# Kernel tuning notes

Hardware: AMD Instinct MI355X
Metric: run time of the kernel (lower is better)

Reference implementation:

```python
import jax, jax.numpy as jnp
import numpy as np

N, FIN, C1, C2 = 4096, 6, 1000, 1000
K1, K2, KR = 3, 6, 3
NR, S, NCLS = 20, 205, 40


def pairwise_adj(x):
    # exp(-squared_euclidean_distance), RGCNN pairwise_distance
    inner = -2.0 * jnp.einsum('bnf,bmf->bnm', x, x)
    sq = jnp.sum(x * x, axis=-1, keepdims=True)
    return jnp.exp(-(sq + inner + jnp.swapaxes(sq, 1, 2)))


def knn_sparsify(adj, k):
    # keep top-k similarities per row, zero the rest (get_one_matrix_knn)
    vals, idx = jax.lax.top_k(adj, k)
    B, n, _ = adj.shape
    b = jnp.arange(B)[:, None, None]
    r = jnp.arange(n)[None, :, None]
    return jnp.zeros_like(adj).at[b, r, idx].set(vals)


def get_laplacian(W):
    # normalized Laplacian L = I - D^-1/2 W D^-1/2
    dinv = 1.0 / jnp.sqrt(jnp.sum(W, axis=-1))
    Lnorm = W * dinv[:, :, None] * dinv[:, None, :]
    return jnp.eye(W.shape[-1], dtype=W.dtype)[None] - Lnorm


def cheb_conv(x, L, W, b, K):
    # Chebyshev recursion: Tx0=x, Tx1=Lx, Txk=2L Tx_{k-1} - Tx_{k-2}
    Tx = [x]
    if K > 1:
        Tx.append(jnp.einsum('bnm,bmf->bnf', L, x))
    for _ in range(2, K):
        Tx.append(2.0 * jnp.einsum('bnm,bmf->bnf', L, Tx[-1]) - Tx[-2])
    xhat = jnp.concatenate(Tx, axis=-1)  # [B, N, K*Fin]
    return jnp.einsum('bnf,fo->bno', xhat, W) + b


def setup_inputs() -> dict:
    key = jax.random.key(0)
    ks = jax.random.split(key, 16)
    sc = 0.02
    return {
        'x': jax.random.normal(ks[0], (1, N, FIN), jnp.float32),
        'k': 40,
        'batch_size': 1,
        'num_points': N,
        'vertices_Reeb': jax.random.normal(ks[1], (NR, 3), jnp.float32),
        'laplacian_Reeb': jax.random.normal(ks[2], (NR, NR), jnp.float32),
        'sccs': jax.random.randint(ks[3], (NR, S), 0, N),
        'W1': jax.random.normal(ks[4], (K1 * FIN, C1), jnp.float32) * sc,
        'b1': jnp.zeros((C1,), jnp.float32),
        'W2': jax.random.normal(ks[5], (K2 * C1, C2), jnp.float32) * sc,
        'b2': jnp.zeros((C2,), jnp.float32),
        'Wr': jax.random.normal(ks[6], (KR * C1, C2), jnp.float32) * sc,
        'br': jnp.zeros((C2,), jnp.float32),
        'fc1_w': jax.random.normal(ks[7], (2 * C2, 512), jnp.float32) * sc,
        'fc1_b': jnp.zeros((512,), jnp.float32),
        'fc2_w': jax.random.normal(ks[8], (512, 128), jnp.float32) * sc,
        'fc2_b': jnp.zeros((128,), jnp.float32),
        'fc3_w': jax.random.normal(ks[9], (128, NCLS), jnp.float32) * sc,
        'fc3_b': jnp.zeros((NCLS,), jnp.float32),
    }


def reference(x, k, batch_size, num_points, vertices_Reeb, laplacian_Reeb, sccs,
              W1, b1, W2, b2, Wr, br, fc1_w, fc1_b, fc2_w, fc2_b, fc3_w, fc3_b):
    fro = lambda a: jnp.linalg.norm(a.reshape(-1))
    regs = []
    # dynamic KNN graph + Laplacian (no_grad in original -> stop_gradient)
    L = jax.lax.stop_gradient(get_laplacian(knn_sparsify(pairwise_adj(x), k)))
    out = jax.nn.relu(cheb_conv(x, L, W1, b1, K1))  # [1, N, 1000]
    regs.append(fro(jnp.einsum('bnc,bnm,bmf->bcf', out, L, x)))
    # Reeb pooling: max over each scc's node features (sample 0)
    vfr = jnp.max(out[0][sccs], axis=1)[None]  # [1, 20, 1000]
    L_reeb = laplacian_Reeb[None]
    # second dynamic graph on features
    L2 = jax.lax.stop_gradient(get_laplacian(knn_sparsify(pairwise_adj(out), k)))
    out2 = jax.nn.relu(cheb_conv(out, L2, W2, b2, K2))
    regs.append(fro(jnp.einsum('bnc,bnm,bmf->bcf', out2, L2, x)))
    out_reeb = jax.nn.relu(cheb_conv(vfr, L_reeb, Wr, br, KR))
    out_m = jnp.max(out2, axis=1)       # [1, 1000]
    reeb_m = jnp.max(out_reeb, axis=1)  # [1, 1000]
    of = jnp.concatenate([reeb_m, out_m], axis=1)  # [1, 2000]
    of = jax.nn.relu(of @ fc1_w + fc1_b)
    regs += [jnp.linalg.norm(fc1_w.T[0]) ** 2, fc1_b[0] ** 2]
    of = jax.nn.relu(of @ fc2_w + fc2_b)
    regs += [jnp.linalg.norm(fc2_w.T[0]) ** 2, fc2_b[0] ** 2]
    of = of @ fc3_w + fc3_b  # [1, 40]
    regs += [jnp.linalg.norm(fc3_w.T[0]) ** 2, fc3_b[0] ** 2]
    return of, jnp.stack(regs)
```

## Files before the change

kernel.cpp:

```cpp
#include <hip/hip_runtime.h>
#include <math.h>

#define N4    4096
#define FDIM  6
#define CC    1000
#define KP    1024
#define KP6   (6 * KP)
#define KNN   40
#define NRB   20
#define SSC   205

typedef __attribute__((ext_vector_type(8))) short bf16x8;
typedef __attribute__((ext_vector_type(4))) float f32x4;

__device__ __forceinline__ unsigned short f2bf(float f) {
    unsigned u = __float_as_uint(f);
    u = (u + 0x7fffu + ((u >> 16) & 1u)) >> 16;
    return (unsigned short)u;
}
__device__ __forceinline__ float bf2f(short s) {
    return __uint_as_float(((unsigned)(unsigned short)s) << 16);
}

__device__ __forceinline__ unsigned d2key(float d) {
    unsigned u = __float_as_uint(d);
    return ((int)u < 0) ? u : (~u) ^ 0x80000000u;
}
__device__ __forceinline__ float key2d(unsigned k) {
    unsigned u = (k >> 31) ? k : (~k) ^ 0x80000000u;
    return __uint_as_float(u);
}

__device__ __forceinline__ void gload16(const unsigned short* g, short* l) {
    __builtin_amdgcn_global_load_lds(
        (const __attribute__((address_space(1))) unsigned int*)g,
        (__attribute__((address_space(3))) unsigned int*)l, 16, 0, 0);
}


__global__ __launch_bounds__(256) void sqx_kernel(const float* __restrict__ x,
                                                  float* __restrict__ sq1,
                                                  float* __restrict__ xhat) {
    int n = blockIdx.x * blockDim.x + threadIdx.x;
    if (n >= N4) return;
    float s = 0.f;
#pragma unroll
    for (int f = 0; f < FDIM; ++f) {
        float v = x[n * FDIM + f];
        s += v * v;
        xhat[n * 18 + f] = v;
    }
    sq1[n] = s;
}


#define NHC 8
#define HSTRIDE 257

struct TopkSh {
    unsigned sv[N4];
    int hist[NHC * HSTRIDE];
    int sc[256];
    float red[8];
    unsigned short cidx[N4];
    unsigned s_pfx;
    int s_need, s_cnt, s_m;
};

__device__ __forceinline__ void hist_pick(TopkSh& sh, int level, int t, int lane, int w, int nc) {
    if (t < 256) {
        int cnt = 0;
        for (int c = 0; c < nc; ++c) cnt += sh.hist[c * HSTRIDE + t];
        sh.sc[t] = cnt;
    }
    __syncthreads();
    if (w == 0) {
        int need = sh.s_need;
        unsigned pfx = sh.s_pfx;
        int c0 = sh.sc[4 * lane + 0], c1 = sh.sc[4 * lane + 1];
        int c2 = sh.sc[4 * lane + 2], c3 = sh.sc[4 * lane + 3];
        int s = c0 + c1 + c2 + c3;
        int suf = s;
#pragma unroll
        for (int off = 1; off < 64; off <<= 1) {
            int ov = __shfl_down(suf, off, 64);
            if (lane + off < 64) suf += ov;
        }
        int above = suf - s;
        int i3 = above + c3, i2 = i3 + c2, i1 = i2 + c1, i0 = i1 + c0;
        if (i3 >= need && i3 - c3 < need) { sh.s_need = need - (i3 - c3); sh.s_pfx = pfx | ((unsigned)(4 * lane + 3) << level); }
        if (i2 >= need && i2 - c2 < need) { sh.s_need = need - (i2 - c2); sh.s_pfx = pfx | ((unsigned)(4 * lane + 2) << level); }
        if (i1 >= need && i1 - c1 < need) { sh.s_need = need - (i1 - c1); sh.s_pfx = pfx | ((unsigned)(4 * lane + 1) << level); }
        if (i0 >= need && i0 - c0 < need) { sh.s_need = need - (i0 - c0); sh.s_pfx = pfx | ((unsigned)(4 * lane + 0) << level); }
    }
    __syncthreads();
}

__device__ void topk_select(TopkSh& sh, int n, int* __restrict__ idx,
                            float* __restrict__ val, float* __restrict__ rowsum) {
    int t = threadIdx.x, lane = t & 63, w = t >> 6;
    if (t == 0) { sh.s_pfx = 0u; sh.s_need = KNN; sh.s_cnt = 0; sh.s_m = 0; }
    for (int q = t; q < NHC * HSTRIDE; q += 512) sh.hist[q] = 0;
    __syncthreads();
    int* hw = &sh.hist[(t & 7) * HSTRIDE];

    {
        unsigned prevb = 0xFFFFFFFFu; int rl = 0;
        for (int i = t; i < N4; i += 512) {
            unsigned b = sh.sv[i] >> 24;
            if (b == prevb) ++rl;
            else { if (rl) atomicAdd(&hw[prevb], rl); prevb = b; rl = 1; }
        }
        if (rl) atomicAdd(&hw[prevb], rl);
    }
    __syncthreads();
    hist_pick(sh, 24, t, lane, w, NHC);
    unsigned b1 = sh.s_pfx >> 24;

    for (int i = t; i < N4; i += 512) {
        unsigned u = sh.sv[i];
        bool isc = ((u >> 24) >= b1);
        unsigned long long mm = __ballot(isc);
        int cw = __popcll(mm);
        int base = 0;
        if (lane == 0 && cw) base = atomicAdd(&sh.s_m, cw);
        base = __shfl(base, 0);
        if (isc) sh.cidx[base + __popcll(mm & ((1ull << lane) - 1ull))] = (unsigned short)i;
    }
    __syncthreads();
    int mcnt = sh.s_m;

    for (int level = 16; level >= 0; level -= 8) {
        for (int q = t; q < HSTRIDE; q += 512) sh.hist[q] = 0;
        __syncthreads();
        unsigned pfx = sh.s_pfx;
        for (int j = t; j < mcnt; j += 512) {
            unsigned u = sh.sv[sh.cidx[j]];
            if ((u >> (level + 8)) == (pfx >> (level + 8)))
                atomicAdd(&sh.hist[(u >> level) & 255], 1);
        }
        __syncthreads();
        hist_pick(sh, level, t, lane, w, 1);
    }
    unsigned Tbits = sh.s_pfx;
    float Tf = __expf(-key2d(Tbits));
    int needEq = sh.s_need;

    float psum = 0.f;
    for (int j = t; j < mcnt; j += 512) {
        unsigned u = sh.sv[sh.cidx[j]];
        if (u > Tbits) {
            int p = atomicAdd(&sh.s_cnt, 1);
            float v = __expf(-key2d(u));
            idx[(size_t)n * KNN + p] = (int)sh.cidx[j];
            val[(size_t)n * KNN + p] = v;
            psum += v;
        }
    }
#pragma unroll
    for (int o = 32; o; o >>= 1) psum += __shfl_down(psum, o);
    if (lane == 0) sh.red[w] = psum;
    __syncthreads();
    if (t == 0) {
        float s = 0.f;
#pragma unroll
        for (int q = 0; q < 8; ++q) s += sh.red[q];
        rowsum[n] = s + (float)needEq * Tf;
    }

    if (t < 64) {
        int filled = KNN - needEq;
        for (int ib = 0; ib < N4 && filled < KNN; ib += 64) {
            bool eq = (sh.sv[ib + t] == Tbits);
            unsigned long long m = __ballot(eq);
            int pre = __popcll(m & ((1ull << t) - 1ull));
            if (eq && (filled + pre) < KNN) {
                idx[(size_t)n * KNN + filled + pre] = ib + t;
                val[(size_t)n * KNN + filled + pre] = Tf;
            }
            filled += __popcll(m);
        }
    }
}

__global__ __launch_bounds__(512) void topk_fused1(const float* __restrict__ x,
                                                   const float* __restrict__ sq1,
                                                   int* __restrict__ idx, float* __restrict__ val,
                                                   float* __restrict__ rowsum) {
    __shared__ TopkSh sh;
    __shared__ float xn[FDIM];
    __shared__ float sns;
    int n = blockIdx.x;
    int t = threadIdx.x;
    if (t < FDIM) xn[t] = x[n * FDIM + t];
    if (t == FDIM) sns = sq1[n];
    __syncthreads();
    float x0 = xn[0], x1 = xn[1], x2 = xn[2], x3 = xn[3], x4 = xn[4], x5 = xn[5];
    float sn = sns;
    for (int i = t; i < N4; i += 512) {
        const float2* xi = (const float2*)(x + i * FDIM);
        float2 p0 = xi[0], p1 = xi[1], p2 = xi[2];
        float d = x0 * p0.x + x1 * p0.y + x2 * p1.x + x3 * p1.y + x4 * p2.x + x5 * p2.y;
        float e = sn + sq1[i] - 2.f * d;
        sh.sv[i] = d2key(e);
    }
    topk_select(sh, n, idx, val, rowsum);
}

__global__ __launch_bounds__(512) void topk_radix(const unsigned short* __restrict__ S,
                                                  int* __restrict__ idx, float* __restrict__ val,
                                                  float* __restrict__ rowsum) {
    __shared__ TopkSh sh;
    int n = blockIdx.x;
    int t = threadIdx.x;
    const unsigned short* row = S + (size_t)n * N4;
    bf16x8 a = *(const bf16x8*)(row + 8 * t);
#pragma unroll
    for (int q = 0; q < 8; ++q) sh.sv[8 * t + q] = d2key(bf2f(a[q]));
    topk_select(sh, n, idx, val, rowsum);
}

__global__ __launch_bounds__(256) void wnorm_kernel(float* __restrict__ wv,
                                                    const int* __restrict__ idx,
                                                    const float* __restrict__ rs) {
    int i = blockIdx.x * 256 + threadIdx.x;
    if (i >= N4 * KNN) return;
    int n = i / KNN;
    wv[i] = wv[i] * rsqrtf(rs[n]) * rsqrtf(rs[idx[i]]);
}

__global__ __launch_bounds__(64) void spmv_cheb(const float* __restrict__ Tc,
                                                const float* __restrict__ Tp,
                                                float* __restrict__ Tn,
                                                const int* __restrict__ idx,
                                                const float* __restrict__ wv,
                                                int F, int sC, int sP, int sN,
                                                float a, float b) {
    __shared__ int   si[KNN];
    __shared__ float sw[KNN];
    int n = blockIdx.x;
    if (threadIdx.x < KNN) {
        si[threadIdx.x] = idx[(size_t)n * KNN + threadIdx.x];
        sw[threadIdx.x] = wv[(size_t)n * KNN + threadIdx.x];
    }
    __syncthreads();
    for (int c = threadIdx.x; c < F; c += blockDim.x) {
        float s = 0.f;
#pragma unroll 8
        for (int j = 0; j < KNN; ++j) s += sw[j] * Tc[(size_t)si[j] * sC + c];
        float v = a * (Tc[(size_t)n * sC + c] - s);
        if (b != 0.f) v -= b * Tp[(size_t)n * sP + c];
        Tn[(size_t)n * sN + c] = v;
    }
}

__global__ __launch_bounds__(256) void spmv_cheb_bf(const unsigned short* __restrict__ Tcbf,
                                                    const unsigned short* __restrict__ Tpbf,
                                                    unsigned short* __restrict__ Tnbf,
                                                    const int* __restrict__ idx,
                                                    const float* __restrict__ wv,
                                                    float a, float b) {
    __shared__ int   si[KNN];
    __shared__ float sw[KNN];
    __shared__ float part[128][8];
    int n = blockIdx.x;
    int t = threadIdx.x;
    int tt = t & 127, h = t >> 7;
    if (t < KNN) {
        si[t] = idx[(size_t)n * KNN + t];
        sw[t] = wv[(size_t)n * KNN + t];
    }
    __syncthreads();
    int c = tt * 8;
    float acc0 = 0, acc1 = 0, acc2 = 0, acc3 = 0, acc4 = 0, acc5 = 0, acc6 = 0, acc7 = 0;
    int j0 = h * 20;
#pragma unroll 4
    for (int j = j0; j < j0 + 20; ++j) {
        bf16x8 v = *(const bf16x8*)(Tcbf + (size_t)si[j] * KP6 + c);
        float wj = sw[j];
        acc0 += wj * bf2f(v[0]); acc1 += wj * bf2f(v[1]);
        acc2 += wj * bf2f(v[2]); acc3 += wj * bf2f(v[3]);
        acc4 += wj * bf2f(v[4]); acc5 += wj * bf2f(v[5]);
        acc6 += wj * bf2f(v[6]); acc7 += wj * bf2f(v[7]);
    }
    if (h == 1) {
        part[tt][0] = acc0; part[tt][1] = acc1; part[tt][2] = acc2; part[tt][3] = acc3;
        part[tt][4] = acc4; part[tt][5] = acc5; part[tt][6] = acc6; part[tt][7] = acc7;
    }
    __syncthreads();
    if (h == 0) {
        acc0 += part[tt][0]; acc1 += part[tt][1]; acc2 += part[tt][2]; acc3 += part[tt][3];
        acc4 += part[tt][4]; acc5 += part[tt][5]; acc6 += part[tt][6]; acc7 += part[tt][7];
        bf16x8 tc = *(const bf16x8*)(Tcbf + (size_t)n * KP6 + c);
        float o0 = a * (bf2f(tc[0]) - acc0), o1 = a * (bf2f(tc[1]) - acc1);
        float o2 = a * (bf2f(tc[2]) - acc2), o3 = a * (bf2f(tc[3]) - acc3);
        float o4 = a * (bf2f(tc[4]) - acc4), o5 = a * (bf2f(tc[5]) - acc5);
        float o6 = a * (bf2f(tc[6]) - acc6), o7 = a * (bf2f(tc[7]) - acc7);
        if (b != 0.f) {
            bf16x8 tp = *(const bf16x8*)(Tpbf + (size_t)n * KP6 + c);
            o0 -= b * bf2f(tp[0]); o1 -= b * bf2f(tp[1]);
            o2 -= b * bf2f(tp[2]); o3 -= b * bf2f(tp[3]);
            o4 -= b * bf2f(tp[4]); o5 -= b * bf2f(tp[5]);
            o6 -= b * bf2f(tp[6]); o7 -= b * bf2f(tp[7]);
        }
        bf16x8 ob;
        ob[0] = (short)f2bf(o0); ob[1] = (short)f2bf(o1);
        ob[2] = (short)f2bf(o2); ob[3] = (short)f2bf(o3);
        ob[4] = (short)f2bf(o4); ob[5] = (short)f2bf(o5);
        ob[6] = (short)f2bf(o6); ob[7] = (short)f2bf(o7);
        *(bf16x8*)(Tnbf + (size_t)n * KP6 + c) = ob;
    }
}


__global__ __launch_bounds__(256) void cvt_bf16_kernel(const float* __restrict__ in,
                                                       unsigned short* __restrict__ out) {
    int i = blockIdx.x * 256 + threadIdx.x;
    int r = i >> 7, g = i & 127;
    bf16x8 v;
    if (g < 125) {
        float4 a = *(const float4*)(in + (size_t)r * CC + g * 8);
        float4 b = *(const float4*)(in + (size_t)r * CC + g * 8 + 4);
        v[0] = (short)f2bf(a.x); v[1] = (short)f2bf(a.y);
        v[2] = (short)f2bf(a.z); v[3] = (short)f2bf(a.w);
        v[4] = (short)f2bf(b.x); v[5] = (short)f2bf(b.y);
        v[6] = (short)f2bf(b.z); v[7] = (short)f2bf(b.w);
    } else {
#pragma unroll
        for (int q = 0; q < 8; ++q) v[q] = 0;
    }
    *(bf16x8*)(out + (size_t)r * KP6 + g * 8) = v;
}

__global__ __launch_bounds__(256) void w2t_kernel(const float* __restrict__ W2,
                                                  unsigned short* __restrict__ out) {
    __shared__ unsigned short tile[64][65];
    int t = threadIdx.x;
    int k0 = blockIdx.x * 64, n0 = blockIdx.y * 64, s = blockIdx.z;
#pragma unroll
    for (int p = 0; p < 16; ++p) {
        int i = p * 256 + t;
        int kk = i >> 6, nn = i & 63;
        int k = k0 + kk, n = n0 + nn;
        float v = (k < CC && n < CC) ? W2[((size_t)s * CC + k) * CC + n] : 0.f;
        tile[kk][nn] = f2bf(v);
    }
    __syncthreads();
#pragma unroll
    for (int p = 0; p < 16; ++p) {
        int i = p * 256 + t;
        int nn = i >> 6, kk = i & 63;
        out[(size_t)(n0 + nn) * KP6 + (size_t)s * KP + k0 + kk] = tile[kk][nn];
    }
}


#define LDT 32
#define SP2 136
#define SP 264
#define ABUF (128 * LDT)
#define BBUF (256 * LDT)

template<int STR>
__device__ __forceinline__ void gemm_core128(const unsigned short* __restrict__ Ag,
                                             const unsigned short* __restrict__ Bg,
                                             short* As, short* Bs, int t,
                                             int kbeg, int kend,
                                             f32x4 (&acc)[4][4]) {
    int l = t & 63, w = t >> 6;
    int wm = (w >> 1) * 64, wn = (w & 1) * 64;
    int lr = l & 15, lq8 = (l >> 4) * 8;
    size_t soff = (size_t)(16 * w + (l >> 2)) * STR + (l & 3) * 8;
    const unsigned short* gA = Ag + soff;
    const unsigned short* gB = Bg + soff;
    int wb = w * 512;
    gload16(gA + kbeg, As + wb);
    gload16(gA + kbeg + (size_t)64 * STR, As + wb + 64 * LDT);
    gload16(gB + kbeg, Bs + wb);
    gload16(gB + kbeg + (size_t)64 * STR, Bs + wb + 64 * LDT);
    __syncthreads();
    int cur = 0;
    for (int k0 = kbeg; k0 < kend; k0 += 32) {
        int nxt = cur ^ 1;
        if (k0 + 32 < kend) {
            short* nA = As + nxt * ABUF + wb;
            short* nB = Bs + nxt * ABUF + wb;
            gload16(gA + k0 + 32, nA);
            gload16(gA + k0 + 32 + (size_t)64 * STR, nA + 64 * LDT);
            gload16(gB + k0 + 32, nB);
            gload16(gB + k0 + 32 + (size_t)64 * STR, nB + 64 * LDT);
        }
        const short* cA = As + cur * ABUF;
        const short* cB = Bs + cur * ABUF;
        bf16x8 af[4], bfr[4];
#pragma unroll
        for (int mi = 0; mi < 4; ++mi)
            af[mi] = *(const bf16x8*)&cA[(wm + mi * 16 + lr) * LDT + lq8];
#pragma unroll
        for (int ni = 0; ni < 4; ++ni)
            bfr[ni] = *(const bf16x8*)&cB[(wn + ni * 16 + lr) * LDT + lq8];
#pragma unroll
        for (int mi = 0; mi < 4; ++mi)
#pragma unroll
            for (int ni = 0; ni < 4; ++ni)
                acc[mi][ni] = __builtin_amdgcn_mfma_f32_16x16x32_bf16(af[mi], bfr[ni], acc[mi][ni], 0, 0, 0);
        __syncthreads();
        cur = nxt;
    }
}

template<int STR>
__device__ __forceinline__ void gemm_core256(const unsigned short* __restrict__ Ag,
                                             const unsigned short* __restrict__ Bg,
                                             short* As, short* Bs, int t,
                                             int kbeg, int kend,
                                             f32x4 (&acc)[4][8]) {
    int l = t & 63, w = t >> 6;
    int wm = (w >> 1) * 64, wn = (w & 1) * 128;
    int lr = l & 15, lq8 = (l >> 4) * 8;
    size_t soff = (size_t)(16 * w + (l >> 2)) * STR + (l & 3) * 8;
    const unsigned short* gA = Ag + soff;
    const unsigned short* gB = Bg + soff;
    int wb = w * 512;
    gload16(gA + kbeg, As + wb);
    gload16(gA + kbeg + (size_t)64 * STR, As + wb + 64 * LDT);
    gload16(gB + kbeg, Bs + wb);
    gload16(gB + kbeg + (size_t)64 * STR, Bs + wb + 64 * LDT);
    gload16(gB + kbeg + (size_t)128 * STR, Bs + wb + 128 * LDT);
    gload16(gB + kbeg + (size_t)192 * STR, Bs + wb + 192 * LDT);
    __syncthreads();
    int cur = 0;
    for (int k0 = kbeg; k0 < kend; k0 += 32) {
        int nxt = cur ^ 1;
        if (k0 + 32 < kend) {
            short* nA = As + nxt * ABUF + wb;
            short* nB = Bs + nxt * BBUF + wb;
            gload16(gA + k0 + 32, nA);
            gload16(gA + k0 + 32 + (size_t)64 * STR, nA + 64 * LDT);
            gload16(gB + k0 + 32, nB);
            gload16(gB + k0 + 32 + (size_t)64 * STR, nB + 64 * LDT);
            gload16(gB + k0 + 32 + (size_t)128 * STR, nB + 128 * LDT);
            gload16(gB + k0 + 32 + (size_t)192 * STR, nB + 192 * LDT);
        }
        const short* cA = As + cur * ABUF;
        const short* cB = Bs + cur * BBUF;
        bf16x8 af[4], bfr[8];
#pragma unroll
        for (int mi = 0; mi < 4; ++mi)
            af[mi] = *(const bf16x8*)&cA[(wm + mi * 16 + lr) * LDT + lq8];
#pragma unroll
        for (int ni = 0; ni < 8; ++ni)
            bfr[ni] = *(const bf16x8*)&cB[(wn + ni * 16 + lr) * LDT + lq8];
#pragma unroll
        for (int mi = 0; mi < 4; ++mi)
#pragma unroll
            for (int ni = 0; ni < 8; ++ni)
                acc[mi][ni] = __builtin_amdgcn_mfma_f32_16x16x32_bf16(af[mi], bfr[ni], acc[mi][ni], 0, 0, 0);
        __syncthreads();
        cur = nxt;
    }
}

__global__ __launch_bounds__(256) void gemm_mfma_big(const unsigned short* __restrict__ A,
                                                     const unsigned short* __restrict__ B,
                                                     unsigned short* __restrict__ Cp) {
    __shared__ short smem[4 * ABUF];
    short* As = smem;
    short* Bs = smem + 2 * ABUF;
    int t = threadIdx.x;
    int m0 = blockIdx.x * 128, n0 = blockIdx.y * 128;
    int kz = blockIdx.z;
    unsigned short* C = Cp + (size_t)kz * N4 * CC;
    f32x4 acc[4][4] = {};
    gemm_core128<KP6>(A + (size_t)m0 * KP6, B + (size_t)n0 * KP6, As, Bs, t,
                      kz * KP, kz * KP + KP, acc);
    int l = t & 63, w = t >> 6;
    int wn = (w & 1) * 64;
    int lr = l & 15, lq4 = (l >> 4) * 4;
    int lrow = (w >> 1) * 16 + lq4;
#pragma unroll
    for (int mi = 0; mi < 4; ++mi) {
        __syncthreads();
#pragma unroll
        for (int ni = 0; ni < 4; ++ni) {
            int col = wn + ni * 16 + lr;
            f32x4 v = acc[mi][ni];
#pragma unroll
            for (int r = 0; r < 4; ++r) smem[(lrow + r) * SP2 + col] = (short)f2bf(v[r]);
        }
        __syncthreads();
#pragma unroll
        for (int q = 0; q < 2; ++q) {
            int row = q * 16 + (t >> 4);
            int col = (t & 15) * 8;
            int gm = m0 + (row >> 4) * 64 + mi * 16 + (row & 15);
            int gn = n0 + col;
            if (gn < CC) {
                bf16x8 vv = *(bf16x8*)&smem[row * SP2 + col];
                *(bf16x8*)(C + (size_t)gm * CC + gn) = vv;
            }
        }
    }
}

__global__ __launch_bounds__(256) void bias_relu_merge(const unsigned short* __restrict__ Cp,
                                                       const float* __restrict__ b2,
                                                       float* __restrict__ out2) {
    size_t i8 = (size_t)blockIdx.x * 256 + threadIdx.x;
    if (i8 >= (size_t)N4 * CC / 8) return;
    size_t i = i8 * 8;
    int c = (int)(i % CC);
    const size_t S = (size_t)N4 * CC;
    float s[8] = {};
#pragma unroll
    for (int z = 0; z < 6; ++z) {
        bf16x8 v = *(const bf16x8*)(Cp + z * S + i);
#pragma unroll
        for (int q = 0; q < 8; ++q) s[q] += bf2f(v[q]);
    }
    float4 o0, o1;
    o0.x = fmaxf(s[0] + b2[c + 0], 0.f); o0.y = fmaxf(s[1] + b2[c + 1], 0.f);
    o0.z = fmaxf(s[2] + b2[c + 2], 0.f); o0.w = fmaxf(s[3] + b2[c + 3], 0.f);
    o1.x = fmaxf(s[4] + b2[c + 4], 0.f); o1.y = fmaxf(s[5] + b2[c + 5], 0.f);
    o1.z = fmaxf(s[6] + b2[c + 6], 0.f); o1.w = fmaxf(s[7] + b2[c + 7], 0.f);
    *(float4*)(out2 + i) = o0;
    *(float4*)(out2 + i + 4) = o1;
}

__global__ __launch_bounds__(256, 2) void gram2_mfma(const unsigned short* __restrict__ Tall,
                                                     const float* __restrict__ sq2,
                                                     unsigned short* __restrict__ S) {
    __shared__ short smem[2 * ABUF + 2 * BBUF];
    short* As = smem;
    short* Bs = smem + 2 * ABUF;
    int t = threadIdx.x;
    int m0 = blockIdx.x * 128, n0 = blockIdx.y * 256;
    f32x4 acc[4][8] = {};
    gemm_core256<KP6>(Tall + (size_t)m0 * KP6, Tall + (size_t)n0 * KP6, As, Bs, t, 0, KP, acc);
    int l = t & 63, w = t >> 6;
    int wn = (w & 1) * 128;
    int lr = l & 15, lq4 = (l >> 4) * 4;
    int lrow = (w >> 1) * 16 + lq4;
#pragma unroll
    for (int mi = 0; mi < 4; ++mi) {
        __syncthreads();
        int mbase = m0 + (w >> 1) * 64 + mi * 16 + lq4;
#pragma unroll
        for (int ni = 0; ni < 8; ++ni) {
            int col = wn + ni * 16 + lr;
            float sn = sq2[n0 + col];
            f32x4 v = acc[mi][ni];
#pragma unroll
            for (int r = 0; r < 4; ++r)
                smem[(lrow + r) * SP + col] = (short)f2bf(sq2[mbase + r] + sn - 2.f * v[r]);
        }
        __syncthreads();
#pragma unroll
        for (int q = 0; q < 4; ++q) {
            int row = q * 8 + (t >> 5);
            int col = (t & 31) * 8;
            int gm = m0 + (row >> 4) * 64 + mi * 16 + (row & 15);
            int gn = n0 + col;
            bf16x8 vv = *(bf16x8*)&smem[row * SP + col];
            *(bf16x8*)(S + (size_t)gm * N4 + gn) = vv;
        }
    }
}


__global__ __launch_bounds__(256) void cheb1_out_kernel(const float* __restrict__ xhat,
                                                        const float* __restrict__ W1,
                                                        const float* __restrict__ b1,
                                                        float* __restrict__ outF) {
    __shared__ float xh[16][18];
    int n0 = blockIdx.x * 16;
    int tid = threadIdx.x;
    for (int i = tid; i < 16 * 18; i += 256) xh[i / 18][i % 18] = xhat[(size_t)n0 * 18 + i];
    __syncthreads();
    for (int c0 = 0; c0 < CC; c0 += 256) {
        int c = c0 + tid;
        if (c < CC) {
            float acc[16];
#pragma unroll
            for (int r = 0; r < 16; ++r) acc[r] = 0.f;
            for (int f = 0; f < 18; ++f) {
                float wv = W1[(size_t)f * CC + c];
#pragma unroll
                for (int r = 0; r < 16; ++r) acc[r] += xh[r][f] * wv;
            }
            float bb = b1[c];
#pragma unroll
            for (int r = 0; r < 16; ++r)
                outF[(size_t)(n0 + r) * CC + c] = fmaxf(acc[r] + bb, 0.f);
        }
    }
}


__global__ __launch_bounds__(256) void matT6_partial(const float* __restrict__ O,
                                                     const float* __restrict__ T, int ts,
                                                     float* __restrict__ M) {
    __shared__ float sT[128][6];
    int t = threadIdx.x;
    int c = blockIdx.x * 256 + t;
    int n0 = blockIdx.y * 128;
    for (int i = t; i < 128 * 6; i += 256) {
        int nn = i / 6, f = i % 6;
        sT[nn][f] = T[(size_t)(n0 + nn) * ts + f];
    }
    __syncthreads();
    if (c >= CC) return;
    float a0 = 0, a1 = 0, a2 = 0, a3 = 0, a4 = 0, a5 = 0;
    for (int nn = 0; nn < 128; ++nn) {
        float o = O[(size_t)(n0 + nn) * CC + c];
        a0 += o * sT[nn][0]; a1 += o * sT[nn][1]; a2 += o * sT[nn][2];
        a3 += o * sT[nn][3]; a4 += o * sT[nn][4]; a5 += o * sT[nn][5];
    }
    atomicAdd(&M[0 * CC + c], a0);
    atomicAdd(&M[1 * CC + c], a1);
    atomicAdd(&M[2 * CC + c], a2);
    atomicAdd(&M[3 * CC + c], a3);
    atomicAdd(&M[4 * CC + c], a4);
    atomicAdd(&M[5 * CC + c], a5);
}

__global__ __launch_bounds__(256) void fro_kernel(const float* __restrict__ M, float* __restrict__ dst) {
    __shared__ float red[256];
    int t = threadIdx.x;
    int i = blockIdx.x * 256 + t;
    float v = (i < 6 * CC) ? M[i] : 0.f;
    red[t] = v * v;
    __syncthreads();
    for (int o = 128; o; o >>= 1) { if (t < o) red[t] += red[t + o]; __syncthreads(); }
    if (t == 0) atomicAdd(dst, red[0]);
}


__global__ __launch_bounds__(256) void vfr_kernel(const float* __restrict__ outF,
                                                  const int* __restrict__ sccs,
                                                  float* __restrict__ vfr) {
    int r = blockIdx.y;
    int c = blockIdx.x * 256 + threadIdx.x;
    if (c >= CC) return;
    int s0 = blockIdx.z * 41;
    float m = 0.f;
    for (int s = s0; s < s0 + 41; ++s) {
        int n = sccs[r * SSC + s];
        m = fmaxf(m, outF[(size_t)n * CC + c]);
    }
    atomicMax((int*)&vfr[(size_t)r * CC + c], __float_as_int(m));
}

__global__ __launch_bounds__(256) void sq2_kernel(const float* __restrict__ outF,
                                                  float* __restrict__ sq2) {
    int lane = threadIdx.x & 63, w = threadIdx.x >> 6;
    int n = blockIdx.x * 4 + w;
    const float* row = outF + (size_t)n * CC;
    float s = 0.f;
    for (int i = lane; i < CC; i += 64) { float v = row[i]; s += v * v; }
#pragma unroll
    for (int o = 32; o; o >>= 1) s += __shfl_down(s, o);
    if (lane == 0) sq2[n] = s;
}

__global__ __launch_bounds__(256) void colmax_kernel(const float* __restrict__ O,
                                                     float* __restrict__ dst) {
    int c = blockIdx.x * 256 + threadIdx.x;
    if (c >= CC) return;
    int n0 = blockIdx.y * 64;
    float m = 0.f;
    for (int n = n0; n < n0 + 64; ++n) m = fmaxf(m, O[(size_t)n * CC + c]);
    atomicMax((int*)&dst[c], __float_as_int(m));
}


__global__ __launch_bounds__(256) void reeb_mm_kernel(const float* __restrict__ Lr,
                                                      const float* __restrict__ Vin,
                                                      const float* __restrict__ Vsub,
                                                      float* __restrict__ Vout, float a2) {
    int c = blockIdx.x * 256 + threadIdx.x;
    if (c >= CC) return;
    int r = blockIdx.y;
    float s = 0.f;
#pragma unroll
    for (int j = 0; j < NRB; ++j) s += Lr[r * NRB + j] * Vin[(size_t)j * CC + c];
    float v = a2 * s;
    if (Vsub) v -= Vsub[(size_t)r * CC + c];
    Vout[(size_t)r * CC + c] = v;
}

#define RKC 25
__global__ __launch_bounds__(256) void reeb_conv_splitk(const float* __restrict__ vfr,
                                                        const float* __restrict__ tr1,
                                                        const float* __restrict__ tr2,
                                                        const float* __restrict__ Wr,
                                                        float* __restrict__ rpre) {
    __shared__ float sA[NRB][RKC];
    int t = threadIdx.x;
    int kbase = blockIdx.y * RKC;
    for (int i = t; i < NRB * RKC; i += 256) {
        int r = i / RKC, kk = i % RKC;
        int kg = kbase + kk;
        float v;
        if (kg < CC)           v = vfr[(size_t)r * CC + kg];
        else if (kg < 2 * CC)  v = tr1[(size_t)r * CC + kg - CC];
        else                   v = tr2[(size_t)r * CC + kg - 2 * CC];
        sA[r][kk] = v;
    }
    __syncthreads();
    int c = blockIdx.x * 256 + t;
    if (c >= CC) return;
    float acc[NRB];
#pragma unroll
    for (int r = 0; r < NRB; ++r) acc[r] = 0.f;
    for (int kk = 0; kk < RKC; ++kk) {
        float wv = Wr[(size_t)(kbase + kk) * CC + c];
#pragma unroll
        for (int r = 0; r < NRB; ++r) acc[r] += sA[r][kk] * wv;
    }
#pragma unroll
    for (int r = 0; r < NRB; ++r) atomicAdd(&rpre[(size_t)r * CC + c], acc[r]);
}

__global__ __launch_bounds__(256) void reeb_max_kernel(const float* __restrict__ pre,
                                                       const float* __restrict__ br,
                                                       float* __restrict__ rbm) {
    int c = blockIdx.x * 256 + threadIdx.x;
    if (c >= CC) return;
    float bb = br[c];
    float m = 0.f;
    for (int r = 0; r < NRB; ++r) m = fmaxf(m, fmaxf(pre[(size_t)r * CC + c] + bb, 0.f));
    rbm[c] = m;
}


__global__ __launch_bounds__(256) void fc1_kernel(const float* __restrict__ rbm,
                                                  const float* __restrict__ otm,
                                                  const float* __restrict__ w,
                                                  float* __restrict__ h1pre) {
    int j = blockIdx.x * 256 + threadIdx.x;
    if (j >= 512) return;
    int i0 = blockIdx.y * 250;
    float s = 0.f;
    for (int i = i0; i < i0 + 250; ++i) {
        float v = (i < CC) ? rbm[i] : otm[i - CC];
        s += v * w[(size_t)i * 512 + j];
    }
    atomicAdd(&h1pre[j], s);
}

__global__ __launch_bounds__(512) void fc23_kernel(const float* __restrict__ h1pre,
                                                   const float* __restrict__ b1f,
                                                   const float* __restrict__ w2,
                                                   const float* __restrict__ b2f,
                                                   const float* __restrict__ w3,
                                                   const float* __restrict__ b3f,
                                                   float* __restrict__ dout) {
    __shared__ float h1[512];
    __shared__ float h2[128];
    int t = threadIdx.x;
    h1[t] = fmaxf(h1pre[t] + b1f[t], 0.f);
    __syncthreads();
    if (t < 128) {
        float s = b2f[t];
        for (int i = 0; i < 512; ++i) s += h1[i] * w2[(size_t)i * 128 + t];
        h2[t] = fmaxf(s, 0.f);
    }
    __syncthreads();
    if (t < 40) {
        float s = b3f[t];
        for (int i = 0; i < 128; ++i) s += h2[i] * w3[(size_t)i * 40 + t];
        dout[t] = s;
    }
}

__global__ __launch_bounds__(256) void finalize_kernel(const float* __restrict__ racc,
                                                       const float* __restrict__ f1w,
                                                       const float* __restrict__ f1b,
                                                       const float* __restrict__ f2w,
                                                       const float* __restrict__ f2b,
                                                       const float* __restrict__ f3w,
                                                       const float* __restrict__ f3b,
                                                       float* __restrict__ dout) {
    __shared__ float red[256];
    __shared__ float res[3];
    int t = threadIdx.x;
    float s1 = 0.f, s2 = 0.f, s3 = 0.f;
    for (int i = t; i < 2000; i += 256) { float v = f1w[(size_t)i * 512]; s1 += v * v; }
    for (int i = t; i < 512; i += 256) { float v = f2w[(size_t)i * 128]; s2 += v * v; }
    if (t < 128) { float v = f3w[(size_t)t * 40]; s3 = v * v; }

    red[t] = s1; __syncthreads();
    for (int o = 128; o; o >>= 1) { if (t < o) red[t] += red[t + o]; __syncthreads(); }
    if (t == 0) res[0] = red[0];
    __syncthreads();
    red[t] = s2; __syncthreads();
    for (int o = 128; o; o >>= 1) { if (t < o) red[t] += red[t + o]; __syncthreads(); }
    if (t == 0) res[1] = red[0];
    __syncthreads();
    red[t] = s3; __syncthreads();
    for (int o = 128; o; o >>= 1) { if (t < o) red[t] += red[t + o]; __syncthreads(); }
    if (t == 0) res[2] = red[0];
    __syncthreads();

    if (t == 0) {
        dout[40] = sqrtf(racc[0]);
        dout[41] = sqrtf(racc[1]);
        dout[42] = res[0];
        dout[43] = f1b[0] * f1b[0];
        dout[44] = res[1];
        dout[45] = f2b[0] * f2b[0];
        dout[46] = res[2];
        dout[47] = f3b[0] * f3b[0];
    }
}


extern "C" void kernel_launch(void* const* d_in, const int* in_sizes, int n_in,
                              void* d_out, int out_size, void* d_ws, size_t ws_size,
                              hipStream_t stream) {
    const float* x    = (const float*)d_in[0];
    const float* Lr   = (const float*)d_in[5];
    const int*   sccs = (const int*)d_in[6];
    const float* W1   = (const float*)d_in[7];
    const float* b1   = (const float*)d_in[8];
    const float* W2   = (const float*)d_in[9];
    const float* b2   = (const float*)d_in[10];
    const float* Wr   = (const float*)d_in[11];
    const float* br   = (const float*)d_in[12];
    const float* f1w  = (const float*)d_in[13];
    const float* f1b  = (const float*)d_in[14];
    const float* f2w  = (const float*)d_in[15];
    const float* f2b  = (const float*)d_in[16];
    const float* f3w  = (const float*)d_in[17];
    const float* f3b  = (const float*)d_in[18];
    float* dout = (float*)d_out;

    char* ws = (char*)d_ws;
    size_t off = 0;
    auto alloc = [&](size_t bytes) -> char* {
        char* p = ws + off;
        off = (off + bytes + 255) & ~(size_t)255;
        return p;
    };
    float* outF = (float*)alloc((size_t)N4 * CC * 4);
    unsigned short* Cpb = (unsigned short*)alloc((size_t)6 * N4 * CC * 2);
    unsigned short* Sb  = (unsigned short*)alloc((size_t)N4 * N4 * 2);
    unsigned short* Tall = (unsigned short*)alloc((size_t)N4 * KP6 * 2);
    unsigned short* W2T6 = Sb;
    float* xhat = (float*)alloc((size_t)N4 * 18 * 4);
    float* sq1  = (float*)alloc(N4 * 4);
    float* sq2  = (float*)alloc(N4 * 4);
    float* rs1  = (float*)alloc(N4 * 4);
    float* rs2  = (float*)alloc(N4 * 4);
    float* wv1  = (float*)alloc((size_t)N4 * KNN * 4);
    float* wv2  = (float*)alloc((size_t)N4 * KNN * 4);
    int*   ix1  = (int*)alloc((size_t)N4 * KNN * 4);
    int*   ix2  = (int*)alloc((size_t)N4 * KNN * 4);
    float* t2x  = (float*)alloc((size_t)N4 * FDIM * 4);
    float* tr1  = (float*)alloc((size_t)NRB * CC * 4);
    float* tr2  = (float*)alloc((size_t)NRB * CC * 4);
    char*  zbase = ws + off;
    float* Mb   = (float*)alloc(6 * CC * 4);
    float* Mb2  = (float*)alloc(6 * CC * 4);
    float* rbm  = (float*)alloc(CC * 4);
    float* otm  = (float*)alloc(CC * 4);
    float* h1p  = (float*)alloc(512 * 4);
    float* racc = (float*)alloc(64 * 4);
    float* rpre = (float*)alloc((size_t)NRB * CC * 4);
    float* vfr  = (float*)alloc((size_t)NRB * CC * 4);
    size_t zlen = (size_t)((ws + off) - zbase);
    if (off > ws_size) return;

    hipMemsetAsync(zbase, 0, zlen, stream);

    sqx_kernel<<<(N4 + 255) / 256, 256, 0, stream>>>(x, sq1, xhat);
    topk_fused1<<<N4, 512, 0, stream>>>(x, sq1, ix1, wv1, rs1);
    wnorm_kernel<<<(N4 * KNN + 255) / 256, 256, 0, stream>>>(wv1, ix1, rs1);

    spmv_cheb<<<N4, 64, 0, stream>>>(xhat, xhat, xhat + 6, ix1, wv1, FDIM, 18, 18, 18, 1.f, 0.f);
    spmv_cheb<<<N4, 64, 0, stream>>>(xhat + 6, xhat, xhat + 12, ix1, wv1, FDIM, 18, 18, 18, 2.f, 1.f);
    cheb1_out_kernel<<<N4 / 16, 256, 0, stream>>>(xhat, W1, b1, outF);

    matT6_partial<<<dim3(4, 32), 256, 0, stream>>>(outF, xhat + 6, 18, Mb);
    fro_kernel<<<24, 256, 0, stream>>>(Mb, racc + 0);

    vfr_kernel<<<dim3(4, NRB, 5), 256, 0, stream>>>(outF, sccs, vfr);

    sq2_kernel<<<N4 / 4, 256, 0, stream>>>(outF, sq2);
    cvt_bf16_kernel<<<N4 * 128 / 256, 256, 0, stream>>>(outF, Tall);
    gram2_mfma<<<dim3(N4 / 128, N4 / 256), 256, 0, stream>>>(Tall, sq2, Sb);
    topk_radix<<<N4, 512, 0, stream>>>(Sb, ix2, wv2, rs2);
    wnorm_kernel<<<(N4 * KNN + 255) / 256, 256, 0, stream>>>(wv2, ix2, rs2);

    w2t_kernel<<<dim3(16, 16, 6), 256, 0, stream>>>(W2, W2T6);

    spmv_cheb<<<N4, 64, 0, stream>>>(x, x, t2x, ix2, wv2, FDIM, FDIM, FDIM, FDIM, 1.f, 0.f);

    spmv_cheb_bf<<<N4, 256, 0, stream>>>(Tall + 0 * KP, Tall + 0 * KP, Tall + 1 * KP, ix2, wv2, 1.f, 0.f);
    spmv_cheb_bf<<<N4, 256, 0, stream>>>(Tall + 1 * KP, Tall + 0 * KP, Tall + 2 * KP, ix2, wv2, 2.f, 1.f);
    spmv_cheb_bf<<<N4, 256, 0, stream>>>(Tall + 2 * KP, Tall + 1 * KP, Tall + 3 * KP, ix2, wv2, 2.f, 1.f);
    spmv_cheb_bf<<<N4, 256, 0, stream>>>(Tall + 3 * KP, Tall + 2 * KP, Tall + 4 * KP, ix2, wv2, 2.f, 1.f);
    spmv_cheb_bf<<<N4, 256, 0, stream>>>(Tall + 4 * KP, Tall + 3 * KP, Tall + 5 * KP, ix2, wv2, 2.f, 1.f);

    gemm_mfma_big<<<dim3(N4 / 128, 8, 6), 256, 0, stream>>>(Tall, W2T6, Cpb);
    bias_relu_merge<<<(int)(((size_t)N4 * CC / 8 + 255) / 256), 256, 0, stream>>>(Cpb, b2, outF);

    matT6_partial<<<dim3(4, 32), 256, 0, stream>>>(outF, t2x, FDIM, Mb2);
    fro_kernel<<<24, 256, 0, stream>>>(Mb2, racc + 1);

    colmax_kernel<<<dim3(4, 64), 256, 0, stream>>>(outF, otm);

    reeb_mm_kernel<<<dim3(4, NRB), 256, 0, stream>>>(Lr, vfr, nullptr, tr1, 1.f);
    reeb_mm_kernel<<<dim3(4, NRB), 256, 0, stream>>>(Lr, tr1, vfr, tr2, 2.f);
    reeb_conv_splitk<<<dim3(4, 120), 256, 0, stream>>>(vfr, tr1, tr2, Wr, rpre);
    reeb_max_kernel<<<4, 256, 0, stream>>>(rpre, br, rbm);

    fc1_kernel<<<dim3(2, 8), 256, 0, stream>>>(rbm, otm, f1w, h1p);
    fc23_kernel<<<1, 512, 0, stream>>>(h1p, f1b, f2w, f2b, f3w, f3b, dout);
    finalize_kernel<<<1, 256, 0, stream>>>(racc, f1w, f1b, f2w, f2b, f3w, f3b, dout);
}
```

Baseline: 686.2 us.

## Use BK=64 single-buffered GEMM core and halve split-K partitions

The big Chebyshev-feature GEMM now loads a 64-wide K slab per iteration into four LDS buffers, with two MFMA passes between barriers, in place of the double-buffered 32-wide prefetch pipeline. Split-K drops from 6 to 3 partitions, so each block covers 2048 of K, and the merge kernel sums only 3 bf16 partials. This cuts partial-sum write and read traffic and halves the barrier count per K. In exchange, global loads no longer overlap compute within a block, and the grid holds half as many blocks.

```diff
diff --git a/kernel.cpp b/kernel.cpp
--- a/kernel.cpp
+++ b/kernel.cpp
@@ -362,50 +362,55 @@
 #define BBUF (256 * LDT)
 
 template<int STR>
-__device__ __forceinline__ void gemm_core128(const unsigned short* __restrict__ Ag,
-                                             const unsigned short* __restrict__ Bg,
-                                             short* As, short* Bs, int t,
-                                             int kbeg, int kend,
-                                             f32x4 (&acc)[4][4]) {
+__device__ __forceinline__ void gemm_core128_bk64(const unsigned short* __restrict__ Ag,
+                                                  const unsigned short* __restrict__ Bg,
+                                                  short* sm, int t,
+                                                  int kbeg, int kend,
+                                                  f32x4 (&acc)[4][4]) {
     int l = t & 63, w = t >> 6;
     int wm = (w >> 1) * 64, wn = (w & 1) * 64;
     int lr = l & 15, lq8 = (l >> 4) * 8;
-    size_t soff = (size_t)(16 * w + (l >> 2)) * STR + (l & 3) * 8;
-    const unsigned short* gA = Ag + soff;
-    const unsigned short* gB = Bg + soff;
-    int wb = w * 512;
-    gload16(gA + kbeg, As + wb);
-    gload16(gA + kbeg + (size_t)64 * STR, As + wb + 64 * LDT);
-    gload16(gB + kbeg, Bs + wb);
-    gload16(gB + kbeg + (size_t)64 * STR, Bs + wb + 64 * LDT);
-    __syncthreads();
-    int cur = 0;
-    for (int k0 = kbeg; k0 < kend; k0 += 32) {
-        int nxt = cur ^ 1;
-        if (k0 + 32 < kend) {
-            short* nA = As + nxt * ABUF + wb;
-            short* nB = Bs + nxt * ABUF + wb;
-            gload16(gA + k0 + 32, nA);
-            gload16(gA + k0 + 32 + (size_t)64 * STR, nA + 64 * LDT);
-            gload16(gB + k0 + 32, nB);
-            gload16(gB + k0 + 32 + (size_t)64 * STR, nB + 64 * LDT);
-        }
-        const short* cA = As + cur * ABUF;
-        const short* cB = Bs + cur * ABUF;
+    short* A0 = sm;
+    short* A1 = sm + ABUF;
+    short* B0 = sm + 2 * ABUF;
+    short* B1 = sm + 3 * ABUF;
+    size_t ga0 = (size_t)(32 * w + (l >> 2)) * STR + (l & 3) * 8;
+    size_t ga1 = ga0 + (size_t)16 * STR;
+    int lo = (32 * w) * LDT;
+    for (int k0 = kbeg; k0 < kend; k0 += 64) {
+        gload16(Ag + ga0 + k0,      A0 + lo);
+        gload16(Ag + ga1 + k0,      A0 + lo + 16 * LDT);
+        gload16(Ag + ga0 + k0 + 32, A1 + lo);
+        gload16(Ag + ga1 + k0 + 32, A1 + lo + 16 * LDT);
+        gload16(Bg + ga0 + k0,      B0 + lo);
+        gload16(Bg + ga1 + k0,      B0 + lo + 16 * LDT);
+        gload16(Bg + ga0 + k0 + 32, B1 + lo);
+        gload16(Bg + ga1 + k0 + 32, B1 + lo + 16 * LDT);
+        __syncthreads();
         bf16x8 af[4], bfr[4];
 #pragma unroll
         for (int mi = 0; mi < 4; ++mi)
-            af[mi] = *(const bf16x8*)&cA[(wm + mi * 16 + lr) * LDT + lq8];
+            af[mi] = *(const bf16x8*)&A0[(wm + mi * 16 + lr) * LDT + lq8];
 #pragma unroll
         for (int ni = 0; ni < 4; ++ni)
-            bfr[ni] = *(const bf16x8*)&cB[(wn + ni * 16 + lr) * LDT + lq8];
+            bfr[ni] = *(const bf16x8*)&B0[(wn + ni * 16 + lr) * LDT + lq8];
+#pragma unroll
+        for (int mi = 0; mi < 4; ++mi)
+#pragma unroll
+            for (int ni = 0; ni < 4; ++ni)
+                acc[mi][ni] = __builtin_amdgcn_mfma_f32_16x16x32_bf16(af[mi], bfr[ni], acc[mi][ni], 0, 0, 0);
+#pragma unroll
+        for (int mi = 0; mi < 4; ++mi)
+            af[mi] = *(const bf16x8*)&A1[(wm + mi * 16 + lr) * LDT + lq8];
+#pragma unroll
+        for (int ni = 0; ni < 4; ++ni)
+            bfr[ni] = *(const bf16x8*)&B1[(wn + ni * 16 + lr) * LDT + lq8];
 #pragma unroll
         for (int mi = 0; mi < 4; ++mi)
 #pragma unroll
             for (int ni = 0; ni < 4; ++ni)
                 acc[mi][ni] = __builtin_amdgcn_mfma_f32_16x16x32_bf16(af[mi], bfr[ni], acc[mi][ni], 0, 0, 0);
         __syncthreads();
-        cur = nxt;
     }
 }
 
@@ -465,15 +470,13 @@
                                                      const unsigned short* __restrict__ B,
                                                      unsigned short* __restrict__ Cp) {
     __shared__ short smem[4 * ABUF];
-    short* As = smem;
-    short* Bs = smem + 2 * ABUF;
     int t = threadIdx.x;
     int m0 = blockIdx.x * 128, n0 = blockIdx.y * 128;
     int kz = blockIdx.z;
     unsigned short* C = Cp + (size_t)kz * N4 * CC;
     f32x4 acc[4][4] = {};
-    gemm_core128<KP6>(A + (size_t)m0 * KP6, B + (size_t)n0 * KP6, As, Bs, t,
-                      kz * KP, kz * KP + KP, acc);
+    gemm_core128_bk64<KP6>(A + (size_t)m0 * KP6, B + (size_t)n0 * KP6, smem, t,
+                           kz * 2 * KP, kz * 2 * KP + 2 * KP, acc);
     int l = t & 63, w = t >> 6;
     int wn = (w & 1) * 64;
     int lr = l & 15, lq4 = (l >> 4) * 4;
@@ -513,7 +516,7 @@
     const size_t S = (size_t)N4 * CC;
     float s[8] = {};
 #pragma unroll
-    for (int z = 0; z < 6; ++z) {
+    for (int z = 0; z < 3; ++z) {
         bf16x8 v = *(const bf16x8*)(Cp + z * S + i);
 #pragma unroll
         for (int q = 0; q < 8; ++q) s[q] += bf2f(v[q]);
@@ -903,7 +906,7 @@
     spmv_cheb_bf<<<N4, 256, 0, stream>>>(Tall + 3 * KP, Tall + 2 * KP, Tall + 4 * KP, ix2, wv2, 2.f, 1.f);
     spmv_cheb_bf<<<N4, 256, 0, stream>>>(Tall + 4 * KP, Tall + 3 * KP, Tall + 5 * KP, ix2, wv2, 2.f, 1.f);
 
-    gemm_mfma_big<<<dim3(N4 / 128, 8, 6), 256, 0, stream>>>(Tall, W2T6, Cpb);
+    gemm_mfma_big<<<dim3(N4 / 128, 8, 3), 256, 0, stream>>>(Tall, W2T6, Cpb);
     bias_relu_merge<<<(int)(((size_t)N4 * CC / 8 + 255) / 256), 256, 0, stream>>>(Cpb, b2, outF);
 
     matT6_partial<<<dim3(4, 32), 256, 0, stream>>>(outF, t2x, FDIM, Mb2);
```

Measured after the change: 665.6 us. 3.0% less time.
